# Performance work log

Measured on AMD Instinct MI355X. Metric: run time of the kernel, lower is better.

The kernel has to match this reference:

```python
import jax, jax.numpy as jnp
import numpy as np

EMBED_DIM = 512
NUM_HEADS = 8
HEAD_DIM = EMBED_DIM // NUM_HEADS
EDGE_DIM = 16
B, N = 2, 2048


def setup_inputs() -> dict:
    key = jax.random.key(0)
    ks = jax.random.split(key, 16)
    s = 1.0 / np.sqrt(EMBED_DIM)
    inp = {
        "x": jax.random.normal(ks[0], (B, N, EMBED_DIM), dtype=jnp.float32),
        "adjacency": jax.random.uniform(ks[1], (B, N, N), dtype=jnp.float32),
        # torch.nn.Linear stores weight as (out, in); we keep that convention
        "Wq": jax.random.uniform(ks[2], (EMBED_DIM, EMBED_DIM), minval=-s, maxval=s),
        "bq": jax.random.uniform(ks[3], (EMBED_DIM,), minval=-s, maxval=s),
        "Wk": jax.random.uniform(ks[4], (EMBED_DIM, EMBED_DIM), minval=-s, maxval=s),
        "bk": jax.random.uniform(ks[5], (EMBED_DIM,), minval=-s, maxval=s),
        "Wv": jax.random.uniform(ks[6], (EMBED_DIM, EMBED_DIM), minval=-s, maxval=s),
        "bv": jax.random.uniform(ks[7], (EMBED_DIM,), minval=-s, maxval=s),
        "Wo": jax.random.uniform(ks[8], (EMBED_DIM, EMBED_DIM), minval=-s, maxval=s),
        "bo": jax.random.uniform(ks[9], (EMBED_DIM,), minval=-s, maxval=s),
        # edge MLP: Linear(1 -> edge_dim) then Linear(edge_dim -> num_heads)
        "We1": jax.random.uniform(ks[10], (EDGE_DIM, 1), minval=-1.0, maxval=1.0),
        "be1": jax.random.uniform(ks[11], (EDGE_DIM,), minval=-1.0, maxval=1.0),
        "We2": jax.random.uniform(ks[12], (NUM_HEADS, EDGE_DIM), minval=-0.25, maxval=0.25),
        "be2": jax.random.uniform(ks[13], (NUM_HEADS,), minval=-0.25, maxval=0.25),
        "edge_bias": jnp.zeros((NUM_HEADS,), dtype=jnp.float32),
    }
    return inp


def reference(x, adjacency, Wq, bq, Wk, bk, Wv, bv, Wo, bo, We1, be1, We2, be2, edge_bias):
    b, n, _ = x.shape
    scale = HEAD_DIM ** (-0.5)

    def split_heads(t):  # (b, n, E) -> (b, H, n, d)
        return t.reshape(b, n, NUM_HEADS, HEAD_DIM).transpose(0, 2, 1, 3)

    q = split_heads(x @ Wq.T + bq)
    k = split_heads(x @ Wk.T + bk)
    v = split_heads(x @ Wv.T + bv)

    # (b, H, n, n)
    attn_scores = jnp.einsum('bhid,bhjd->bhij', q, k) * scale

    # edge MLP applied pointwise to each adjacency entry: 1 -> edge_dim -> num_heads
    # hidden: (b, n, n, edge_dim)
    hidden = jax.nn.relu(adjacency[..., None] * We1[:, 0] + be1)
    edge_attn = jnp.einsum('bijE,hE->bhij', hidden, We2) + be2[None, :, None, None]

    boost = adjacency[:, None, :, :] * edge_bias[None, :, None, None]
    attn_scores = attn_scores + edge_attn + boost

    attn_probs = jax.nn.softmax(attn_scores, axis=-1)
    out = jnp.einsum('bhij,bhjd->bhid', attn_probs, v)
    out = out.transpose(0, 2, 1, 3).reshape(b, n, EMBED_DIM)
    out = out @ Wo.T + bo
    return out
```

## Files before the change

### kernel.cpp

```cpp
#include <hip/hip_runtime.h>
#include <stdint.h>


#define SEQ 2048
#define EMB 512
#define NH  8
#define HD  64
#define NB  2
#define L2E 1.4426950408889634f

typedef unsigned int   u32;
typedef unsigned short u16;
typedef u32   u32x4  __attribute__((ext_vector_type(4)));
typedef float f32x4  __attribute__((ext_vector_type(4)));
typedef float f32x2  __attribute__((ext_vector_type(2)));
typedef __bf16 bf16x8 __attribute__((ext_vector_type(8)));

#define MFMA16(a, b, c) __builtin_amdgcn_mfma_f32_16x16x32_bf16((a), (b), (c), 0, 0, 0)

static __device__ __forceinline__ u16 f2bf(float f) {
  return __builtin_bit_cast(u16, (__bf16)f);
}
static __device__ __forceinline__ u32 pack2(float a, float b) {
  return (u32)f2bf(a) | ((u32)f2bf(b) << 16);
}
static __device__ __forceinline__ bf16x8 ldfrag(const u16* p) {
  return __builtin_bit_cast(bf16x8, *(const u32x4*)p);
}
static __device__ __forceinline__ void glds16(const u16* g, u16* l) {
  __builtin_amdgcn_global_load_lds(
      (const __attribute__((address_space(1))) u32*)(const void*)g,
      (__attribute__((address_space(3))) u32*)(void*)l, 16, 0, 0);
}
static __device__ __forceinline__ u32 comb2(u32 a, u32 d, float rl) {
  float lo = __builtin_bit_cast(float, a << 16)
           + __builtin_bit_cast(float, d << 16);
  float hi = __builtin_bit_cast(float, a & 0xffff0000u)
           + __builtin_bit_cast(float, d & 0xffff0000u);
  return pack2(lo * rl, hi * rl);
}
static __device__ __forceinline__ u32x4 comb4(u32x4 a, u32x4 d, float rl) {
  u32x4 r;
  r[0] = comb2(a[0], d[0], rl); r[1] = comb2(a[1], d[1], rl);
  r[2] = comb2(a[2], d[2], rl); r[3] = comb2(a[3], d[3], rl);
  return r;
}


__global__ void prep_kernel(const float* __restrict__ x,
                            const float* __restrict__ Wq, const float* __restrict__ Wk,
                            const float* __restrict__ Wv, const float* __restrict__ Wo,
                            const float* __restrict__ We1, const float* __restrict__ be1,
                            const float* __restrict__ We2, const float* __restrict__ be2,
                            const float* __restrict__ ebias,
                            u16* __restrict__ xb, u16* __restrict__ wqkv,
                            u16* __restrict__ wob, float* __restrict__ co) {
  const int blk = blockIdx.x, tid = threadIdx.x;
  if (blk < 2048) {
    int i = (blk * 256 + tid) * 4;
    float4 v = *(const float4*)(x + i);
    *(uint2*)(xb + i) = make_uint2(pack2(v.x, v.y), pack2(v.z, v.w));
  } else if (blk < 3072) {
    int i = ((blk - 2048) * 256 + tid) * 4;
    int m = i >> 18;
    int off = i & 262143;
    const float* src = (m == 0) ? Wq : ((m == 1) ? Wk : ((m == 2) ? Wv : Wo));
    u16* dst = (m < 3) ? (wqkv + (size_t)m * 262144) : wob;
    float4 v = *(const float4*)(src + off);
    *(uint2*)(dst + off) = make_uint2(pack2(v.x, v.y), pack2(v.z, v.w));
  } else {
    const int e = tid & 15, h = tid >> 4;
    if (tid < 128) {
      co[49 + e * 8 + h] = 0.0f;
      if (h == 0) { co[17 + e] = 0.0f; co[33 + e] = 0.0f; }
    }
    __syncthreads();
    if (tid < 128) {
      float w1 = We1[e], b1 = be1[e], w2 = We2[h * 16 + e];
      float u0 = b1, u1 = w1 + b1;
      bool on  = (u0 >= 0.0f) && (u1 >= 0.0f);
      bool off = (u0 <= 0.0f) && (u1 <= 0.0f);
      bool crossing = (!on) && (!off);
      float ca = on ? (w2 * b1) : (crossing ? 0.5f * w2 * b1 : 0.0f);
      float cb = on ? (w2 * w1) : (crossing ? 0.5f * w2 * w1 : 0.0f);
      #pragma unroll
      for (int d = 1; d < 16; d <<= 1) { ca += __shfl_xor(ca, d); cb += __shfl_xor(cb, d); }
      if (e == 0) { co[h] = (be2[h] + ca) * L2E; co[8 + h] = (ebias[h] + cb) * L2E; }
      unsigned long long msk = __ballot(crossing);
      int midx = __popcll(msk & 0xFFFFull & ((1ull << e) - 1ull));
      int mcnt = __popcll(msk & 0xFFFFull);
      if (crossing) {
        co[49 + midx * 8 + h] = 0.5f * w2 * L2E;
        if (h == 0) { co[17 + midx] = w1; co[33 + midx] = b1; }
      }
      if (tid == 0) ((int*)co)[16] = mcnt;
    }
  }
}

#define LDB 72
__global__ __launch_bounds__(256) void gemm_qkv_kernel(
    const u16* __restrict__ A, const u16* __restrict__ Bm,
    const float* __restrict__ bq, const float* __restrict__ bk, const float* __restrict__ bv,
    u16* __restrict__ qh, u16* __restrict__ ksw, u16* __restrict__ vsw)
{
  __shared__ u16 sm[64 * LDB + 128 * LDB];
  u16* As = sm;
  u16* Bs = sm + 64 * LDB;
  const int tid = threadIdx.x;
  const int lane = tid & 63, w = tid >> 6;
  const int q = lane >> 4, l15 = lane & 15;
  const int m0 = blockIdx.y * 64;
  const int n0 = blockIdx.x * 128;

  f32x4 acc[4][2];
  f32x4 zero = {0.f, 0.f, 0.f, 0.f};
  #pragma unroll
  for (int i = 0; i < 4; i++) { acc[i][0] = zero; acc[i][1] = zero; }

  const int ar = tid >> 2, aq = tid & 3;
  const int br = tid >> 1, bh = tid & 1;
  const u16* ga = A  + (size_t)(m0 + ar) * EMB + aq * 16;
  const u16* gb = Bm + (size_t)(n0 + br) * EMB + bh * 32;
  u16* la = &As[ar * LDB + aq * 16];
  u16* lb = &Bs[br * LDB + bh * 32];

  u32x4 a0, a1, b0, b1, b2, b3;
  a0 = *(const u32x4*)(ga);      a1 = *(const u32x4*)(ga + 8);
  b0 = *(const u32x4*)(gb);      b1 = *(const u32x4*)(gb + 8);
  b2 = *(const u32x4*)(gb + 16); b3 = *(const u32x4*)(gb + 24);
  ga += 64; gb += 64;

  for (int k0 = 0; k0 < EMB; k0 += 64) {
    __syncthreads();
    *(u32x4*)(la) = a0;      *(u32x4*)(la + 8) = a1;
    *(u32x4*)(lb) = b0;      *(u32x4*)(lb + 8) = b1;
    *(u32x4*)(lb + 16) = b2; *(u32x4*)(lb + 24) = b3;
    __syncthreads();
    if (k0 + 64 < EMB) {
      a0 = *(const u32x4*)(ga);      a1 = *(const u32x4*)(ga + 8);
      b0 = *(const u32x4*)(gb);      b1 = *(const u32x4*)(gb + 8);
      b2 = *(const u32x4*)(gb + 16); b3 = *(const u32x4*)(gb + 24);
      ga += 64; gb += 64;
    }
    bf16x8 af[4][2], bfr[2][2];
    #pragma unroll
    for (int mi = 0; mi < 4; mi++)
      #pragma unroll
      for (int kk = 0; kk < 2; kk++)
        af[mi][kk] = ldfrag(&As[(mi*16 + l15) * LDB + kk*32 + q*8]);
    #pragma unroll
    for (int ni = 0; ni < 2; ni++)
      #pragma unroll
      for (int kk = 0; kk < 2; kk++)
        bfr[ni][kk] = ldfrag(&Bs[(w*32 + ni*16 + l15) * LDB + kk*32 + q*8]);
    #pragma unroll
    for (int mi = 0; mi < 4; mi++)
      #pragma unroll
      for (int ni = 0; ni < 2; ni++)
        #pragma unroll
        for (int kk = 0; kk < 2; kk++)
          acc[mi][ni] = MFMA16(af[mi][kk], bfr[ni][kk], acc[mi][ni]);
  }

  const int mat = n0 >> 9;
  const float* bias = (mat == 0) ? bq : ((mat == 1) ? bk : bv);
  const float mul = (mat == 0) ? 0.125f * L2E : 1.0f;
  const int b_ = m0 >> 11;
  const int nbase = m0 & 2047;

  #pragma unroll
  for (int p = 0; p < 2; p++) {
    __syncthreads();
    if ((w >> 1) == p) {
      #pragma unroll
      for (int ni = 0; ni < 2; ni++) {
        const int dd = (w & 1) * 32 + ni * 16 + l15;
        const float bsv = bias[(n0 & 511) + (w * 32 + ni * 16 + l15)];
        #pragma unroll
        for (int mi = 0; mi < 4; mi++) {
          #pragma unroll
          for (int r = 0; r < 4; r++) {
            const int nr = mi * 16 + q * 4 + r;
            const float val = (acc[mi][ni][r] + bsv) * mul;
            int idx;
            if (mat == 0)      idx = nr * 64 + dd;
            else if (mat == 1) idx = (nr >> 4) * 1024 + ((dd >> 5) << 9)
                                   + ((((dd >> 3) & 3) * 16 + (nr & 15)) << 3) + (dd & 7);
            else               idx = ((dd >> 4) << 10) + (((nr >> 5) & 1) << 9)
                                   + ((((nr >> 3) & 3) * 16 + (dd & 15)) << 3) + (nr & 7);
            sm[idx] = f2bf(val);
          }
        }
      }
    }
    __syncthreads();
    const int hh = ((n0 & 511) >> 6) + p;
    u16* gdst;
    if (mat == 0)      gdst = qh  + ((size_t)(b_ * NH + hh) * SEQ + nbase) * HD;
    else if (mat == 1) gdst = ksw + (size_t)(b_ * NH + hh) * 131072 + (nbase >> 4) * 1024;
    else               gdst = vsw + (size_t)(b_ * NH + hh) * 131072 + (nbase >> 6) * 4096;
    *(u32x4*)(gdst + tid * 16)     = *(const u32x4*)(sm + tid * 16);
    *(u32x4*)(gdst + tid * 16 + 8) = *(const u32x4*)(sm + tid * 16 + 8);
  }
}

__global__ __launch_bounds__(256) void gemm_out_kernel(
    const u16* __restrict__ om0, const u16* __restrict__ om1,
    const float* __restrict__ lsp, const u16* __restrict__ Bm,
    const float* __restrict__ bo, float* __restrict__ out)
{
  __shared__ u16 As[64 * LDB];
  __shared__ u16 Bs[64 * LDB];
  const int tid = threadIdx.x;
  const int lane = tid & 63, w = tid >> 6;
  const int q = lane >> 4, l15 = lane & 15;
  const int m0 = blockIdx.y * 64;
  const int n0 = blockIdx.x * 64;

  f32x4 acc[4];
  f32x4 zero = {0.f, 0.f, 0.f, 0.f};
  #pragma unroll
  for (int i = 0; i < 4; i++) acc[i] = zero;

  const int ar = tid >> 2, aq = tid & 3;
  const int arow = m0 + ar;
  const int libase = (arow >> 11) * 16384 + (arow & 2047);
  const u16* ga0 = om0 + (size_t)arow * EMB + aq * 16;
  const u16* ga1 = om1 + (size_t)arow * EMB + aq * 16;
  const u16* gb  = Bm + (size_t)(n0 + ar) * EMB + aq * 16;
  u16* la = &As[ar * LDB + aq * 16];
  u16* lb = &Bs[ar * LDB + aq * 16];

  u32x4 a0, a1, d0, d1, b0, b1;
  float rl;
  a0 = *(const u32x4*)(ga0); a1 = *(const u32x4*)(ga0 + 8);
  d0 = *(const u32x4*)(ga1); d1 = *(const u32x4*)(ga1 + 8);
  b0 = *(const u32x4*)(gb);  b1 = *(const u32x4*)(gb + 8);
  rl = 1.0f / (lsp[libase] + lsp[32768 + libase]);
  ga0 += 64; ga1 += 64; gb += 64;

  for (int k0 = 0; k0 < EMB; k0 += 64) {
    __syncthreads();
    *(u32x4*)(la)     = comb4(a0, d0, rl);
    *(u32x4*)(la + 8) = comb4(a1, d1, rl);
    *(u32x4*)(lb) = b0; *(u32x4*)(lb + 8) = b1;
    __syncthreads();
    if (k0 + 64 < EMB) {
      const int h = (k0 + 64) >> 6;
      a0 = *(const u32x4*)(ga0); a1 = *(const u32x4*)(ga0 + 8);
      d0 = *(const u32x4*)(ga1); d1 = *(const u32x4*)(ga1 + 8);
      b0 = *(const u32x4*)(gb);  b1 = *(const u32x4*)(gb + 8);
      rl = 1.0f / (lsp[libase + h * 2048] + lsp[32768 + libase + h * 2048]);
      ga0 += 64; ga1 += 64; gb += 64;
    }
    bf16x8 af[4][2], bfr[2];
    #pragma unroll
    for (int mi = 0; mi < 4; mi++)
      #pragma unroll
      for (int kk = 0; kk < 2; kk++)
        af[mi][kk] = ldfrag(&As[(mi*16 + l15) * LDB + kk*32 + q*8]);
    #pragma unroll
    for (int kk = 0; kk < 2; kk++)
      bfr[kk] = ldfrag(&Bs[(w*16 + l15) * LDB + kk*32 + q*8]);
    #pragma unroll
    for (int mi = 0; mi < 4; mi++)
      #pragma unroll
      for (int kk = 0; kk < 2; kk++)
        acc[mi] = MFMA16(af[mi][kk], bfr[kk], acc[mi]);
  }

  int col = n0 + w*16 + l15;
  float bsv = bo[col];
  #pragma unroll
  for (int mi = 0; mi < 4; mi++) {
    int rowb = m0 + mi*16 + q*4;
    #pragma unroll
    for (int r = 0; r < 4; r++)
      out[(size_t)(rowb + r) * EMB + col] = acc[mi][r] + bsv;
  }
}

template<int MT>
struct FlashCtx {
  const u16 *kgp, *vgp;
  const float* arow;
  bf16x8 qf0, qf1;
  float Ah, Bh;
  f32x2 Ah2, Bh2;
  float ctr[(MT > 8) ? MT : 1], dtr[(MT > 8) ? MT : 1], wtr[(MT > 8) ? MT : 1];
  f32x2 ctr2[(MT <= 8) ? MT : 1], dtr2[(MT <= 8) ? MT : 1], wtr2[(MT <= 8) ? MT : 1];
  int lane, w, q, l15, pxor;
};

template<int MT>
static __device__ __forceinline__ void flash_stage(const FlashCtx<MT>& c,
                                                   u16* Kb, u16* Vb, int it) {
  const int o = c.w * 1024 + c.lane * 8;
  const u16* kg = c.kgp + it * 4096;
  const u16* vg = c.vgp + it * 4096;
  glds16(kg + o,       Kb + o);
  glds16(kg + o + 512, Kb + o + 512);
  glds16(vg + o,       Vb + o);
  glds16(vg + o + 512, Vb + o + 512);
}

template<int MT>
static __device__ __forceinline__ void flash_iter(
    const FlashCtx<MT>& c, int it, int tend, u16* Kb, u16* Vb, u16* nKb, u16* nVb,
    u16* psw, float4* avc, float4* avn, f32x4* O, float& lsum)
{
  __syncthreads();
  if (it + 1 < tend) flash_stage(c, nKb, nVb, it + 1);
  const int nx = (it + 1 < tend) ? it + 1 : tend - 1;
  #pragma unroll
  for (int jt = 0; jt < 4; jt++)
    avn[jt] = *(const float4*)(c.arow + nx * 64 + jt * 16);
  __builtin_amdgcn_sched_barrier(0);

  f32x4 zero = {0.f, 0.f, 0.f, 0.f};
  const int lo = c.lane * 8;

  f32x4 S[4];
  #pragma unroll
  for (int jt = 0; jt < 4; jt++) {
    bf16x8 kf0 = ldfrag(Kb + jt * 1024 + lo);
    bf16x8 kf1 = ldfrag(Kb + jt * 1024 + 512 + lo);
    f32x4 s = MFMA16(kf0, c.qf0, zero);
    S[jt] = MFMA16(kf1, c.qf1, s);
  }

  #pragma unroll
  for (int half = 0; half < 2; half++) {
    #pragma unroll
    for (int jj = 0; jj < 2; jj++) {
      const int jt = half * 2 + jj;
      float p[4];
      if constexpr (MT <= 8) {
        const float* av = (const float*)&avc[jt];
        f32x2 a01 = {av[0], av[1]};
        f32x2 a23 = {av[2], av[3]};
        f32x2 e01 = __builtin_elementwise_fma(a01, c.Bh2, c.Ah2);
        f32x2 e23 = __builtin_elementwise_fma(a23, c.Bh2, c.Ah2);
        #pragma unroll
        for (int t = 0; t < MT; t++) {
          f32x2 u01 = __builtin_elementwise_fma(a01, c.ctr2[t], c.dtr2[t]);
          f32x2 u23 = __builtin_elementwise_fma(a23, c.ctr2[t], c.dtr2[t]);
          u01 = __builtin_elementwise_max(u01, -u01);
          u23 = __builtin_elementwise_max(u23, -u23);
          e01 = __builtin_elementwise_fma(u01, c.wtr2[t], e01);
          e23 = __builtin_elementwise_fma(u23, c.wtr2[t], e23);
        }
        f32x2 s01 = {S[jt][0], S[jt][1]};
        f32x2 s23 = {S[jt][2], S[jt][3]};
        s01 += e01; s23 += e23;
        p[0] = __builtin_amdgcn_exp2f(s01.x);
        p[1] = __builtin_amdgcn_exp2f(s01.y);
        p[2] = __builtin_amdgcn_exp2f(s23.x);
        p[3] = __builtin_amdgcn_exp2f(s23.y);
      } else {
        #pragma unroll
        for (int r = 0; r < 4; r++) {
          float a = ((const float*)&avc[jt])[r];
          float e = fmaf(a, c.Bh, c.Ah);
          #pragma unroll
          for (int t = 0; t < MT; t++)
            e = fmaf(fabsf(fmaf(a, c.ctr[t], c.dtr[t])), c.wtr[t], e);
          p[r] = __builtin_amdgcn_exp2f(S[jt][r] + e);
        }
      }
      lsum += (p[0] + p[1]) + (p[2] + p[3]);
      *(uint2*)(psw + ((c.l15 * 64 + jt * 16 + c.q * 4) ^ c.pxor)) =
          make_uint2(pack2(p[0], p[1]), pack2(p[2], p[3]));
    }
    bf16x8 pf = ldfrag(psw + ((c.l15 * 64 + half * 32 + c.q * 8) ^ c.pxor));
    #pragma unroll
    for (int dt = 0; dt < 4; dt++) {
      bf16x8 vf = ldfrag(Vb + dt * 1024 + half * 512 + lo);
      O[dt] = MFMA16(vf, pf, O[dt]);
    }
  }
}

template<int MT>
__device__ __forceinline__ void flash_body(
    u16* Kb0, u16* Kb1, u16* Vb0, u16* Vb1, u16* Pb,
    const u16* __restrict__ qh, const u16* __restrict__ ksw, const u16* __restrict__ vsw,
    const float* __restrict__ adj, const float* __restrict__ coeff,
    u16* __restrict__ om0, u16* __restrict__ om1, float* __restrict__ lsp)
{
  const int tid = threadIdx.x, lane = tid & 63, w = tid >> 6;
  const int q = lane >> 4, l15 = lane & 15;
  const int i0 = blockIdx.x * 64;
  const int h = blockIdx.y;
  const int b = blockIdx.z >> 1, jh = blockIdx.z & 1;
  const int t0 = jh * 16, tend = t0 + 16;
  const int bh = b * NH + h;
  const int iw = i0 + w * 16;

  FlashCtx<MT> c;
  c.lane = lane; c.w = w; c.q = q; c.l15 = l15;
  c.pxor = (l15 & 7) << 3;
  if constexpr (MT <= 8) {
    c.Ah2 = (f32x2){coeff[h], coeff[h]};
    c.Bh2 = (f32x2){coeff[8 + h], coeff[8 + h]};
    #pragma unroll
    for (int t = 0; t < MT; t++) {
      float cv = coeff[17 + t], dv = coeff[33 + t], wv = coeff[49 + t * 8 + h];
      c.ctr2[t] = (f32x2){cv, cv};
      c.dtr2[t] = (f32x2){dv, dv};
      c.wtr2[t] = (f32x2){wv, wv};
    }
  } else {
    c.Ah = coeff[h]; c.Bh = coeff[8 + h];
    #pragma unroll
    for (int t = 0; t < MT; t++) {
      c.ctr[t] = coeff[17 + t];
      c.dtr[t] = coeff[33 + t];
      c.wtr[t] = coeff[49 + t * 8 + h];
    }
  }
  const u16* qrow = qh + ((size_t)bh * SEQ + iw + l15) * HD;
  c.qf0 = ldfrag(qrow + q * 8);
  c.qf1 = ldfrag(qrow + 32 + q * 8);
  c.kgp = ksw + (size_t)bh * 131072;
  c.vgp = vsw + (size_t)bh * 131072;
  c.arow = adj + ((size_t)b * SEQ + iw + l15) * SEQ + q * 4;

  f32x4 O[4];
  f32x4 zero = {0.f, 0.f, 0.f, 0.f};
  #pragma unroll
  for (int dt = 0; dt < 4; dt++) O[dt] = zero;
  float lsum = 0.0f;

  u16* psw = Pb + w * 1024;

  flash_stage(c, Kb0, Vb0, t0);
  float4 avA[4], avB[4];
  #pragma unroll
  for (int jt = 0; jt < 4; jt++)
    avA[jt] = *(const float4*)(c.arow + t0 * 64 + jt * 16);

  #pragma unroll 1
  for (int it2 = t0; it2 < tend; it2 += 2) {
    flash_iter(c, it2,     tend, Kb0, Vb0, Kb1, Vb1, psw, avA, avB, O, lsum);
    flash_iter(c, it2 + 1, tend, Kb1, Vb1, Kb0, Vb0, psw, avB, avA, O, lsum);
  }

  lsum += __shfl_xor(lsum, 16);
  lsum += __shfl_xor(lsum, 32);
  if (lane < 16)
    lsp[(size_t)jh * 32768 + (size_t)bh * SEQ + iw + l15] = lsum;

  u16* orow = (jh ? om1 : om0)
            + ((size_t)b * SEQ + iw + l15) * EMB + h * HD + q * 4;
  #pragma unroll
  for (int dt = 0; dt < 4; dt++)
    *(uint2*)(orow + dt * 16) = make_uint2(pack2(O[dt][0], O[dt][1]),
                                           pack2(O[dt][2], O[dt][3]));
}

__global__ __launch_bounds__(256, 4) void flash_kernel(
    const u16* __restrict__ qh, const u16* __restrict__ ksw, const u16* __restrict__ vsw,
    const float* __restrict__ adj, const float* __restrict__ coeff,
    u16* __restrict__ om0, u16* __restrict__ om1, float* __restrict__ lsp)
{
  __shared__ __align__(16) u16 Kb[2][4096];
  __shared__ __align__(16) u16 Vb[2][4096];
  __shared__ __align__(16) u16 Pb[4096];
  const int mt = ((const int*)coeff)[16];
  if (mt <= 4)
    flash_body<4>(Kb[0], Kb[1], Vb[0], Vb[1], Pb, qh, ksw, vsw, adj, coeff, om0, om1, lsp);
  else if (mt <= 8)
    flash_body<8>(Kb[0], Kb[1], Vb[0], Vb[1], Pb, qh, ksw, vsw, adj, coeff, om0, om1, lsp);
  else
    flash_body<16>(Kb[0], Kb[1], Vb[0], Vb[1], Pb, qh, ksw, vsw, adj, coeff, om0, om1, lsp);
}

extern "C" void kernel_launch(void* const* d_in, const int* in_sizes, int n_in,
                              void* d_out, int out_size, void* d_ws, size_t ws_size,
                              hipStream_t stream) {
  const float* x     = (const float*)d_in[0];
  const float* adj   = (const float*)d_in[1];
  const float* Wq    = (const float*)d_in[2];
  const float* bq    = (const float*)d_in[3];
  const float* Wk    = (const float*)d_in[4];
  const float* bk    = (const float*)d_in[5];
  const float* Wv    = (const float*)d_in[6];
  const float* bv    = (const float*)d_in[7];
  const float* Wo    = (const float*)d_in[8];
  const float* bo    = (const float*)d_in[9];
  const float* We1   = (const float*)d_in[10];
  const float* be1   = (const float*)d_in[11];
  const float* We2   = (const float*)d_in[12];
  const float* be2   = (const float*)d_in[13];
  const float* ebias = (const float*)d_in[14];
  float* out = (float*)d_out;

  char* ws = (char*)d_ws;
  u16*   xb   = (u16*)(ws + 0);
  u16*   wqkv = (u16*)(ws + 4194304);
  u16*   wob  = (u16*)(ws + 5767168);
  u16*   qh   = (u16*)(ws + 6291456);
  u16*   ksw  = (u16*)(ws + 10485760);
  u16*   vsw  = (u16*)(ws + 14680064);
  u16*   om0  = (u16*)(ws + 18874368);
  float* co   = (float*)(ws + 23068672);
  u16*   om1  = xb;
  float* lsp  = (float*)wqkv;
  if (ws_size < 23069696) return;

  prep_kernel<<<3073, 256, 0, stream>>>(x, Wq, Wk, Wv, Wo, We1, be1, We2, be2, ebias,
                                        xb, wqkv, wob, co);
  gemm_qkv_kernel<<<dim3(12, 64), 256, 0, stream>>>(xb, wqkv, bq, bk, bv, qh, ksw, vsw);
  flash_kernel<<<dim3(32, NH, NB * 2), 256, 0, stream>>>(qh, ksw, vsw, adj, co,
                                                         om0, om1, lsp);
  gemm_out_kernel<<<dim3(8, 64), 256, 0, stream>>>(om0, om1, lsp, wob, bo, out);
}
```

Baseline: 184.5 us.

## Split flash key tiles across waves and keep P in registers via 16x16x16 MFMA

Reorganizes the flash attention kernel so each wave handles all 64 query rows of the block but only a 16-key slice of each 64-key tile, rather than 16 query rows across all keys. Because the S accumulator layout now matches the B operand of the 16x16x16 bf16 MFMA, probabilities feed the PV product directly from registers, removing the shared-memory P round trip. Partial O and row sums are then reduced across the four waves through shared memory at the end. The cost is a much larger register footprint (16 O accumulators and 8 Q fragments), so launch bounds drop to 2 blocks per SIMD, plus extra barriers and the cross-wave reduction.

```diff
diff --git a/kernel.cpp b/kernel.cpp
--- a/kernel.cpp
+++ b/kernel.cpp
@@ -15,8 +15,25 @@
 typedef float f32x4  __attribute__((ext_vector_type(4)));
 typedef float f32x2  __attribute__((ext_vector_type(2)));
 typedef __bf16 bf16x8 __attribute__((ext_vector_type(8)));
+typedef __bf16 bf16x4 __attribute__((ext_vector_type(4)));
+typedef short  s16x4  __attribute__((ext_vector_type(4)));
 
 #define MFMA16(a, b, c) __builtin_amdgcn_mfma_f32_16x16x32_bf16((a), (b), (c), 0, 0, 0)
+
+static __device__ __forceinline__ f32x4 pv16(uint2 a, uint2 b, f32x4 c) {
+#if defined(__HIP_DEVICE_COMPILE__)
+#if __has_builtin(__builtin_amdgcn_mfma_f32_16x16x16bf16_1k)
+  return __builtin_amdgcn_mfma_f32_16x16x16bf16_1k(
+      __builtin_bit_cast(s16x4, a), __builtin_bit_cast(s16x4, b), c, 0, 0, 0);
+#else
+  return __builtin_amdgcn_mfma_f32_16x16x16_bf16(
+      __builtin_bit_cast(bf16x4, a), __builtin_bit_cast(bf16x4, b), c, 0, 0, 0);
+#endif
+#else
+  (void)a; (void)b;
+  return c;
+#endif
+}
 
 static __device__ __forceinline__ u16 f2bf(float f) {
   return __builtin_bit_cast(u16, (__bf16)f);
@@ -284,13 +301,13 @@
 template<int MT>
 struct FlashCtx {
   const u16 *kgp, *vgp;
-  const float* arow;
-  bf16x8 qf0, qf1;
+  const float* arow[4];
+  bf16x8 qf[4][2];
   float Ah, Bh;
   f32x2 Ah2, Bh2;
   float ctr[(MT > 8) ? MT : 1], dtr[(MT > 8) ? MT : 1], wtr[(MT > 8) ? MT : 1];
   f32x2 ctr2[(MT <= 8) ? MT : 1], dtr2[(MT <= 8) ? MT : 1], wtr2[(MT <= 8) ? MT : 1];
-  int lane, w, q, l15, pxor;
+  int lane, w, q, l15, vbase;
 };
 
 template<int MT>
@@ -308,83 +325,81 @@
 template<int MT>
 static __device__ __forceinline__ void flash_iter(
     const FlashCtx<MT>& c, int it, int tend, u16* Kb, u16* Vb, u16* nKb, u16* nVb,
-    u16* psw, float4* avc, float4* avn, f32x4* O, float& lsum)
+    float4* avc, float4* avn, f32x4 (*O)[4], float* lsum)
 {
   __syncthreads();
   if (it + 1 < tend) flash_stage(c, nKb, nVb, it + 1);
-  const int nx = (it + 1 < tend) ? it + 1 : tend - 1;
-  #pragma unroll
-  for (int jt = 0; jt < 4; jt++)
-    avn[jt] = *(const float4*)(c.arow + nx * 64 + jt * 16);
+  const int nx = (it + 1 < tend) ? it + 1 : it;
+  #pragma unroll
+  for (int g = 0; g < 4; g++)
+    avn[g] = *(const float4*)(c.arow[g] + nx * 64);
   __builtin_amdgcn_sched_barrier(0);
 
   f32x4 zero = {0.f, 0.f, 0.f, 0.f};
-  const int lo = c.lane * 8;
-
+
+  bf16x8 kf0 = ldfrag(Kb + c.w * 1024 + c.lane * 8);
+  bf16x8 kf1 = ldfrag(Kb + c.w * 1024 + 512 + c.lane * 8);
   f32x4 S[4];
   #pragma unroll
-  for (int jt = 0; jt < 4; jt++) {
-    bf16x8 kf0 = ldfrag(Kb + jt * 1024 + lo);
-    bf16x8 kf1 = ldfrag(Kb + jt * 1024 + 512 + lo);
-    f32x4 s = MFMA16(kf0, c.qf0, zero);
-    S[jt] = MFMA16(kf1, c.qf1, s);
-  }
-
-  #pragma unroll
-  for (int half = 0; half < 2; half++) {
-    #pragma unroll
-    for (int jj = 0; jj < 2; jj++) {
-      const int jt = half * 2 + jj;
-      float p[4];
-      if constexpr (MT <= 8) {
-        const float* av = (const float*)&avc[jt];
-        f32x2 a01 = {av[0], av[1]};
-        f32x2 a23 = {av[2], av[3]};
-        f32x2 e01 = __builtin_elementwise_fma(a01, c.Bh2, c.Ah2);
-        f32x2 e23 = __builtin_elementwise_fma(a23, c.Bh2, c.Ah2);
+  for (int g = 0; g < 4; g++) {
+    f32x4 s = MFMA16(kf0, c.qf[g][0], zero);
+    S[g] = MFMA16(kf1, c.qf[g][1], s);
+  }
+
+  uint2 pa[4];
+  #pragma unroll
+  for (int g = 0; g < 4; g++) {
+    float p0, p1, p2, p3;
+    if constexpr (MT <= 8) {
+      const float* av = (const float*)&avc[g];
+      f32x2 a01 = {av[0], av[1]};
+      f32x2 a23 = {av[2], av[3]};
+      f32x2 e01 = __builtin_elementwise_fma(a01, c.Bh2, c.Ah2);
+      f32x2 e23 = __builtin_elementwise_fma(a23, c.Bh2, c.Ah2);
+      #pragma unroll
+      for (int t = 0; t < MT; t++) {
+        f32x2 u01 = __builtin_elementwise_fma(a01, c.ctr2[t], c.dtr2[t]);
+        f32x2 u23 = __builtin_elementwise_fma(a23, c.ctr2[t], c.dtr2[t]);
+        u01 = __builtin_elementwise_max(u01, -u01);
+        u23 = __builtin_elementwise_max(u23, -u23);
+        e01 = __builtin_elementwise_fma(u01, c.wtr2[t], e01);
+        e23 = __builtin_elementwise_fma(u23, c.wtr2[t], e23);
+      }
+      p0 = __builtin_amdgcn_exp2f(S[g][0] + e01.x);
+      p1 = __builtin_amdgcn_exp2f(S[g][1] + e01.y);
+      p2 = __builtin_amdgcn_exp2f(S[g][2] + e23.x);
+      p3 = __builtin_amdgcn_exp2f(S[g][3] + e23.y);
+    } else {
+      float pp[4];
+      #pragma unroll
+      for (int r = 0; r < 4; r++) {
+        float a = ((const float*)&avc[g])[r];
+        float e = fmaf(a, c.Bh, c.Ah);
         #pragma unroll
-        for (int t = 0; t < MT; t++) {
-          f32x2 u01 = __builtin_elementwise_fma(a01, c.ctr2[t], c.dtr2[t]);
-          f32x2 u23 = __builtin_elementwise_fma(a23, c.ctr2[t], c.dtr2[t]);
-          u01 = __builtin_elementwise_max(u01, -u01);
-          u23 = __builtin_elementwise_max(u23, -u23);
-          e01 = __builtin_elementwise_fma(u01, c.wtr2[t], e01);
-          e23 = __builtin_elementwise_fma(u23, c.wtr2[t], e23);
-        }
-        f32x2 s01 = {S[jt][0], S[jt][1]};
-        f32x2 s23 = {S[jt][2], S[jt][3]};
-        s01 += e01; s23 += e23;
-        p[0] = __builtin_amdgcn_exp2f(s01.x);
-        p[1] = __builtin_amdgcn_exp2f(s01.y);
-        p[2] = __builtin_amdgcn_exp2f(s23.x);
-        p[3] = __builtin_amdgcn_exp2f(s23.y);
-      } else {
-        #pragma unroll
-        for (int r = 0; r < 4; r++) {
-          float a = ((const float*)&avc[jt])[r];
-          float e = fmaf(a, c.Bh, c.Ah);
-          #pragma unroll
-          for (int t = 0; t < MT; t++)
-            e = fmaf(fabsf(fmaf(a, c.ctr[t], c.dtr[t])), c.wtr[t], e);
-          p[r] = __builtin_amdgcn_exp2f(S[jt][r] + e);
-        }
+        for (int t = 0; t < MT; t++)
+          e = fmaf(fabsf(fmaf(a, c.ctr[t], c.dtr[t])), c.wtr[t], e);
+        pp[r] = __builtin_amdgcn_exp2f(S[g][r] + e);
       }
-      lsum += (p[0] + p[1]) + (p[2] + p[3]);
-      *(uint2*)(psw + ((c.l15 * 64 + jt * 16 + c.q * 4) ^ c.pxor)) =
-          make_uint2(pack2(p[0], p[1]), pack2(p[2], p[3]));
-    }
-    bf16x8 pf = ldfrag(psw + ((c.l15 * 64 + half * 32 + c.q * 8) ^ c.pxor));
-    #pragma unroll
-    for (int dt = 0; dt < 4; dt++) {
-      bf16x8 vf = ldfrag(Vb + dt * 1024 + half * 512 + lo);
-      O[dt] = MFMA16(vf, pf, O[dt]);
-    }
-  }
+      p0 = pp[0]; p1 = pp[1]; p2 = pp[2]; p3 = pp[3];
+    }
+    lsum[g] += (p0 + p1) + (p2 + p3);
+    pa[g] = make_uint2(pack2(p0, p1), pack2(p2, p3));
+  }
+
+  uint2 vfr[4];
+  #pragma unroll
+  for (int dt = 0; dt < 4; dt++)
+    vfr[dt] = *(const uint2*)(Vb + c.vbase + dt * 1024);
+  #pragma unroll
+  for (int g = 0; g < 4; g++)
+    #pragma unroll
+    for (int dt = 0; dt < 4; dt++)
+      O[g][dt] = pv16(vfr[dt], pa[g], O[g][dt]);
 }
 
 template<int MT>
 __device__ __forceinline__ void flash_body(
-    u16* Kb0, u16* Kb1, u16* Vb0, u16* Vb1, u16* Pb,
+    u16* Kb0, u16* Kb1, u16* Vb0, u16* Vb1, float* lsb,
     const u16* __restrict__ qh, const u16* __restrict__ ksw, const u16* __restrict__ vsw,
     const float* __restrict__ adj, const float* __restrict__ coeff,
     u16* __restrict__ om0, u16* __restrict__ om1, float* __restrict__ lsp)
@@ -396,11 +411,10 @@
   const int b = blockIdx.z >> 1, jh = blockIdx.z & 1;
   const int t0 = jh * 16, tend = t0 + 16;
   const int bh = b * NH + h;
-  const int iw = i0 + w * 16;
 
   FlashCtx<MT> c;
   c.lane = lane; c.w = w; c.q = q; c.l15 = l15;
-  c.pxor = (l15 & 7) << 3;
+  c.vbase = ((w >> 1) & 1) * 512 + ((w * 2 + (q >> 1)) & 3) * 128 + l15 * 8 + (q & 1) * 4;
   if constexpr (MT <= 8) {
     c.Ah2 = (f32x2){coeff[h], coeff[h]};
     c.Bh2 = (f32x2){coeff[8 + h], coeff[8 + h]};
@@ -420,61 +434,120 @@
       c.wtr[t] = coeff[49 + t * 8 + h];
     }
   }
-  const u16* qrow = qh + ((size_t)bh * SEQ + iw + l15) * HD;
-  c.qf0 = ldfrag(qrow + q * 8);
-  c.qf1 = ldfrag(qrow + 32 + q * 8);
+  const u16* qbase = qh + ((size_t)bh * SEQ + i0 + l15) * HD + q * 8;
+  #pragma unroll
+  for (int g = 0; g < 4; g++) {
+    c.qf[g][0] = ldfrag(qbase + g * 16 * HD);
+    c.qf[g][1] = ldfrag(qbase + g * 16 * HD + 32);
+    c.arow[g] = adj + ((size_t)b * SEQ + i0 + g * 16 + l15) * SEQ + w * 16 + q * 4;
+  }
   c.kgp = ksw + (size_t)bh * 131072;
   c.vgp = vsw + (size_t)bh * 131072;
-  c.arow = adj + ((size_t)b * SEQ + iw + l15) * SEQ + q * 4;
-
-  f32x4 O[4];
+
+  f32x4 O[4][4];
   f32x4 zero = {0.f, 0.f, 0.f, 0.f};
   #pragma unroll
-  for (int dt = 0; dt < 4; dt++) O[dt] = zero;
-  float lsum = 0.0f;
-
-  u16* psw = Pb + w * 1024;
+  for (int g = 0; g < 4; g++)
+    #pragma unroll
+    for (int dt = 0; dt < 4; dt++) O[g][dt] = zero;
+  float lsum[4] = {0.f, 0.f, 0.f, 0.f};
 
   flash_stage(c, Kb0, Vb0, t0);
   float4 avA[4], avB[4];
   #pragma unroll
-  for (int jt = 0; jt < 4; jt++)
-    avA[jt] = *(const float4*)(c.arow + t0 * 64 + jt * 16);
+  for (int g = 0; g < 4; g++)
+    avA[g] = *(const float4*)(c.arow[g] + t0 * 64);
 
   #pragma unroll 1
   for (int it2 = t0; it2 < tend; it2 += 2) {
-    flash_iter(c, it2,     tend, Kb0, Vb0, Kb1, Vb1, psw, avA, avB, O, lsum);
-    flash_iter(c, it2 + 1, tend, Kb1, Vb1, Kb0, Vb0, psw, avB, avA, O, lsum);
-  }
-
-  lsum += __shfl_xor(lsum, 16);
-  lsum += __shfl_xor(lsum, 32);
-  if (lane < 16)
-    lsp[(size_t)jh * 32768 + (size_t)bh * SEQ + iw + l15] = lsum;
-
-  u16* orow = (jh ? om1 : om0)
-            + ((size_t)b * SEQ + iw + l15) * EMB + h * HD + q * 4;
-  #pragma unroll
-  for (int dt = 0; dt < 4; dt++)
-    *(uint2*)(orow + dt * 16) = make_uint2(pack2(O[dt][0], O[dt][1]),
-                                           pack2(O[dt][2], O[dt][3]));
-}
-
-__global__ __launch_bounds__(256, 4) void flash_kernel(
+    flash_iter(c, it2,     tend, Kb0, Vb0, Kb1, Vb1, avA, avB, O, lsum);
+    flash_iter(c, it2 + 1, tend, Kb1, Vb1, Kb0, Vb0, avB, avA, O, lsum);
+  }
+
+  #pragma unroll
+  for (int g = 0; g < 4; g++) {
+    lsum[g] += __shfl_xor(lsum[g], 16);
+    lsum[g] += __shfl_xor(lsum[g], 32);
+  }
+
+  float* redA = (float*)Kb0;
+  float* redB = (float*)Vb0;
+  __syncthreads();
+  if (w == 1) {
+    #pragma unroll
+    for (int g = 0; g < 4; g++)
+      #pragma unroll
+      for (int dt = 0; dt < 4; dt++)
+        *(f32x4*)(redA + ((g * 4 + dt) * 64 + lane) * 4) = O[g][dt];
+  } else if (w == 3) {
+    #pragma unroll
+    for (int g = 0; g < 4; g++)
+      #pragma unroll
+      for (int dt = 0; dt < 4; dt++)
+        *(f32x4*)(redB + ((g * 4 + dt) * 64 + lane) * 4) = O[g][dt];
+  }
+  if (lane < 16) {
+    #pragma unroll
+    for (int g = 0; g < 4; g++) lsb[w * 64 + g * 16 + lane] = lsum[g];
+  }
+  __syncthreads();
+  if (w == 0) {
+    #pragma unroll
+    for (int g = 0; g < 4; g++)
+      #pragma unroll
+      for (int dt = 0; dt < 4; dt++)
+        O[g][dt] += *(const f32x4*)(redA + ((g * 4 + dt) * 64 + lane) * 4);
+  } else if (w == 2) {
+    #pragma unroll
+    for (int g = 0; g < 4; g++)
+      #pragma unroll
+      for (int dt = 0; dt < 4; dt++)
+        O[g][dt] += *(const f32x4*)(redB + ((g * 4 + dt) * 64 + lane) * 4);
+  }
+  __syncthreads();
+  if (w == 2) {
+    #pragma unroll
+    for (int g = 0; g < 4; g++)
+      #pragma unroll
+      for (int dt = 0; dt < 4; dt++)
+        *(f32x4*)(redA + ((g * 4 + dt) * 64 + lane) * 4) = O[g][dt];
+  }
+  __syncthreads();
+  if (w == 0) {
+    #pragma unroll
+    for (int g = 0; g < 4; g++)
+      #pragma unroll
+      for (int dt = 0; dt < 4; dt++)
+        O[g][dt] += *(const f32x4*)(redA + ((g * 4 + dt) * 64 + lane) * 4);
+    float t = lsb[lane] + lsb[64 + lane] + lsb[128 + lane] + lsb[192 + lane];
+    lsp[(size_t)jh * 32768 + (size_t)bh * SEQ + i0 + lane] = t;
+    u16* ob = (jh ? om1 : om0) + ((size_t)b * SEQ + i0) * EMB + h * HD;
+    #pragma unroll
+    for (int g = 0; g < 4; g++)
+      #pragma unroll
+      for (int dt = 0; dt < 4; dt++) {
+        u16* orow = ob + (size_t)(g * 16 + l15) * EMB + dt * 16 + q * 4;
+        *(uint2*)orow = make_uint2(pack2(O[g][dt][0], O[g][dt][1]),
+                                   pack2(O[g][dt][2], O[g][dt][3]));
+      }
+  }
+}
+
+__global__ __launch_bounds__(256, 2) void flash_kernel(
     const u16* __restrict__ qh, const u16* __restrict__ ksw, const u16* __restrict__ vsw,
     const float* __restrict__ adj, const float* __restrict__ coeff,
     u16* __restrict__ om0, u16* __restrict__ om1, float* __restrict__ lsp)
 {
   __shared__ __align__(16) u16 Kb[2][4096];
   __shared__ __align__(16) u16 Vb[2][4096];
-  __shared__ __align__(16) u16 Pb[4096];
+  __shared__ __align__(16) float lsb[256];
   const int mt = ((const int*)coeff)[16];
   if (mt <= 4)
-    flash_body<4>(Kb[0], Kb[1], Vb[0], Vb[1], Pb, qh, ksw, vsw, adj, coeff, om0, om1, lsp);
+    flash_body<4>(Kb[0], Kb[1], Vb[0], Vb[1], lsb, qh, ksw, vsw, adj, coeff, om0, om1, lsp);
   else if (mt <= 8)
-    flash_body<8>(Kb[0], Kb[1], Vb[0], Vb[1], Pb, qh, ksw, vsw, adj, coeff, om0, om1, lsp);
+    flash_body<8>(Kb[0], Kb[1], Vb[0], Vb[1], lsb, qh, ksw, vsw, adj, coeff, om0, om1, lsp);
   else
-    flash_body<16>(Kb[0], Kb[1], Vb[0], Vb[1], Pb, qh, ksw, vsw, adj, coeff, om0, om1, lsp);
+    flash_body<16>(Kb[0], Kb[1], Vb[0], Vb[1], lsb, qh, ksw, vsw, adj, coeff, om0, om1, lsp);
 }
 
 extern "C" void kernel_launch(void* const* d_in, const int* in_sizes, int n_in,
```

Result: slower. 197.8 us (+7.2%).
